# Kernel tuning notes

Measured on AMD Instinct MI355X. Metric: run time of the kernel, lower is better.

Reference implementation:

```python
import jax, jax.numpy as jnp
import numpy as np

N_NODES = 9
NEG_SLOPE = 0.2
# static edge list from the module (src, dst) pairs, PyG convention row0=src, row1=dst
_E = np.array([[0,1],[1,0],[0,3],[3,0],[0,5],[5,0],[0,7],[7,0],
               [1,2],[2,1],[3,4],[4,3],[5,6],[6,5],[7,8],[8,7]], dtype=np.int32).T
# GATv2Conv default add_self_loops=True
SRC = jnp.asarray(np.concatenate([_E[0], np.arange(N_NODES, dtype=np.int32)]))
DST = jnp.asarray(np.concatenate([_E[1], np.arange(N_NODES, dtype=np.int32)]))


def setup_inputs() -> dict:
    key = jax.random.key(0)
    k1, k2, k3, k4 = jax.random.split(key, 4)
    B, C_IN, C_OUT = 16384, 256, 256
    scale = 1.0 / np.sqrt(C_IN)
    return {
        "x": jax.random.normal(k1, (B, N_NODES, C_IN), jnp.float32),
        "W_l": jax.random.normal(k2, (C_IN, C_OUT), jnp.float32) * scale,
        "W_r": jax.random.normal(k3, (C_IN, C_OUT), jnp.float32) * scale,
        "att": jax.random.normal(k4, (C_OUT,), jnp.float32) * scale,
        "bias": jnp.zeros((C_OUT,), jnp.float32),
    }


def reference(x, W_l, W_r, att, bias):
    # x: [B, N, C_in] batch of identical small graphs
    xl = jnp.einsum("bnc,cd->bnd", x, W_l)  # source-side projection
    xr = jnp.einsum("bnc,cd->bnd", x, W_r)  # target-side projection
    # per-edge GATv2 score: a^T LeakyReLU(x_l[src] + x_r[dst])
    e = jax.nn.leaky_relu(xl[:, SRC] + xr[:, DST], NEG_SLOPE)  # [B, E, C_out]
    score = jnp.einsum("bed,d->be", e, att)                    # [B, E]
    # softmax over incoming edges of each destination node (segment softmax)
    sT = score.T                                               # [E, B]
    m = jax.ops.segment_max(sT, DST, num_segments=N_NODES)     # [N, B]
    ex = jnp.exp(sT - m[DST])
    denom = jax.ops.segment_sum(ex, DST, num_segments=N_NODES)
    alpha = ex / denom[DST]                                    # [E, B]
    # scatter-aggregate messages alpha * x_l[src] into dst
    msg = xl[:, SRC] * alpha.T[..., None]                      # [B, E, C_out]
    out = jax.ops.segment_sum(msg.transpose(1, 0, 2), DST, num_segments=N_NODES)
    return out.transpose(1, 0, 2) + bias                       # [B, N, C_out]
```

## Files before the change

### kernel.cpp

```cpp
#include <hip/hip_runtime.h>
#include <hip/hip_bf16.h>

typedef __attribute__((ext_vector_type(8))) short short8;
typedef __attribute__((ext_vector_type(4))) float f32x4;
typedef __attribute__((ext_vector_type(4))) unsigned short u16x4;

#define STAGE_BYTES (144 * 512)
#define PART_OFF    0
#define ALPHA_OFF   (8 * 25 * 16 * 4)
#define LDS_BYTES   STAGE_BYTES

__device__ __forceinline__ unsigned short f2bf(float f) {
    unsigned int u = __float_as_uint(f);
    unsigned int r = (u + 0x7fffu + ((u >> 16) & 1u)) >> 16;
    return (unsigned short)r;
}

constexpr int C_SRC[25] = {0,1,0,3,0,5,0,7,1,2,3,4,5,6,7,8, 0,1,2,3,4,5,6,7,8};
constexpr int C_DST[25] = {1,0,3,0,5,0,7,0,2,1,4,3,6,5,8,7, 0,1,2,3,4,5,6,7,8};
constexpr int C_NINC[9]  = {5,3,2,3,2,3,2,3,2};
constexpr int C_IOFF[9]  = {0,5,8,10,13,15,18,20,23};
constexpr int C_INCE[25] = {1,3,5,7,16, 0,9,17, 8,18, 2,11,19, 10,20, 4,13,21, 12,22, 6,15,23, 14,24};
constexpr int C_INCS[25] = {1,3,5,7,0,  0,2,1,  1,2,  0,4,3,  3,4,  0,6,5,  5,6,  0,8,7,  7,8};
__device__ const int D_NINC[9]  = {5,3,2,3,2,3,2,3,2};
__device__ const int D_IOFF[9]  = {0,5,8,10,13,15,18,20,23};
__device__ const int D_INCE[25] = {1,3,5,7,16, 0,9,17, 8,18, 2,11,19, 10,20, 4,13,21, 12,22, 6,15,23, 14,24};

__global__ void convert_w_kernel(const float* __restrict__ Wl,
                                 const float* __restrict__ Wr,
                                 unsigned short* __restrict__ WT) {
    int n = blockIdx.x;
    int k = threadIdx.x;
    float v = (n < 256) ? Wl[k * 256 + n] : Wr[k * 256 + (n - 256)];
    WT[n * 256 + k] = f2bf(v);
}

__global__ __launch_bounds__(512, 2) void gat_fused_kernel(
        const float* __restrict__ x,
        const unsigned short* __restrict__ WT,
        const float* __restrict__ att,
        const float* __restrict__ bias,
        float* __restrict__ out) {
    __shared__ __align__(16) char smem[LDS_BYTES];
    float* partials = (float*)(smem + PART_OFF);
    float* alphas   = (float*)(smem + ALPHA_OFF);

    const int tid  = threadIdx.x;
    const int lane = tid & 63;
    const int w    = tid >> 6;
    const int gl   = lane >> 4;
    const int li   = lane & 15;
    const int blk  = blockIdx.x;

    const int c0 = 32 * w + li, c1 = c0 + 16;
    const float attc0 = att[c0], attc1 = att[c1];
    const float bc0   = bias[c0], bc1 = bias[c1];

    const float* xblk = x + (size_t)blk * 36864;
    {
        f32x4 xv[18];
        #pragma unroll
        for (int it = 0; it < 18; ++it)
            xv[it] = *(const f32x4*)(xblk + it * 2048 + tid * 4);
        #pragma unroll
        for (int it = 0; it < 18; ++it) {
            int f    = it * 2048 + tid * 4;
            int gr   = f >> 8;
            int c    = f & 255;
            int g    = gr / 9;
            int node = gr - g * 9;
            int srow = node * 16 + g;
            u16x4 pk = { f2bf(xv[it][0]), f2bf(xv[it][1]), f2bf(xv[it][2]), f2bf(xv[it][3]) };
            *(u16x4*)(smem + srow * 512 + ((2 * c) ^ (g << 4))) = pk;
        }
    }
    __syncthreads();

    const f32x4 ZERO = {0.f, 0.f, 0.f, 0.f};
    f32x4 aL[9][2], aR[9][2];
    #pragma unroll
    for (int m = 0; m < 9; ++m) {
        aL[m][0] = ZERO; aL[m][1] = ZERO; aR[m][0] = ZERO; aR[m][1] = ZERO;
    }
    const unsigned short* WL0 = WT + (size_t)((32 * w + li) * 256 + gl * 8);
    const unsigned short* WL1 = WL0 + 16 * 256;
    const unsigned short* WR0 = WL0 + 256 * 256;
    const unsigned short* WR1 = WR0 + 16 * 256;

    #pragma unroll
    for (int kc = 0; kc < 8; ++kc) {
        short8 bl0 = *(const short8*)(WL0 + kc * 32);
        short8 bl1 = *(const short8*)(WL1 + kc * 32);
        short8 br0 = *(const short8*)(WR0 + kc * 32);
        short8 br1 = *(const short8*)(WR1 + kc * 32);
        const int inner = ((kc * 64) + (gl * 16)) ^ (li << 4);
        short8 am[9];
        #pragma unroll
        for (int m = 0; m < 9; ++m)
            am[m] = *(const short8*)(smem + (m * 16 + li) * 512 + inner);
        #pragma unroll
        for (int m = 0; m < 9; ++m) {
            aL[m][0] = __builtin_amdgcn_mfma_f32_16x16x32_bf16(am[m], bl0, aL[m][0], 0, 0, 0);
            aL[m][1] = __builtin_amdgcn_mfma_f32_16x16x32_bf16(am[m], bl1, aL[m][1], 0, 0, 0);
            aR[m][0] = __builtin_amdgcn_mfma_f32_16x16x32_bf16(am[m], br0, aR[m][0], 0, 0, 0);
            aR[m][1] = __builtin_amdgcn_mfma_f32_16x16x32_bf16(am[m], br1, aR[m][1], 0, 0, 0);
        }
    }
    __syncthreads();

    #pragma unroll
    for (int e = 0; e < 25; ++e) {
        const int s = C_SRC[e], d = C_DST[e];
        float p0 = 0.f, p1 = 0.f, p2 = 0.f, p3 = 0.f;
        #pragma unroll
        for (int nt = 0; nt < 2; ++nt) {
            const float ac = nt ? attc1 : attc0;
            #pragma unroll
            for (int r = 0; r < 4; ++r) {
                float v  = aL[s][nt][r] + aR[d][nt][r];
                float lr = fmaxf(v, 0.2f * v);
                float t  = ac * lr;
                if (r == 0) p0 += t; else if (r == 1) p1 += t;
                else if (r == 2) p2 += t; else p3 += t;
            }
        }
        #pragma unroll
        for (int m = 1; m < 16; m <<= 1) {
            p0 += __shfl_xor(p0, m);
            p1 += __shfl_xor(p1, m);
            p2 += __shfl_xor(p2, m);
            p3 += __shfl_xor(p3, m);
        }
        if (li == 0) {
            f32x4 pk = {p0, p1, p2, p3};
            *(f32x4*)(partials + (w * 25 + e) * 16 + 4 * gl) = pk;
        }
    }
    __syncthreads();

    if (tid < 144) {
        int n = tid >> 4, g = tid & 15;
        int off = D_IOFF[n], cnt = D_NINC[n];
        float mx = -1e30f;
        for (int i = 0; i < cnt; ++i) {
            int e = D_INCE[off + i];
            float s = 0.f;
            #pragma unroll
            for (int ww = 0; ww < 8; ++ww) s += partials[(ww * 25 + e) * 16 + g];
            alphas[e * 16 + g] = s;
            mx = fmaxf(mx, s);
        }
        float ssum = 0.f;
        for (int i = 0; i < cnt; ++i)
            ssum += __expf(alphas[D_INCE[off + i] * 16 + g] - mx);
        float inv = 1.f / ssum;
        for (int i = 0; i < cnt; ++i) {
            int e = D_INCE[off + i];
            alphas[e * 16 + g] = __expf(alphas[e * 16 + g] - mx) * inv;
        }
    }
    __syncthreads();

    #pragma unroll
    for (int n = 0; n < 9; ++n) {
        f32x4 o0 = {bc0, bc0, bc0, bc0};
        f32x4 o1 = {bc1, bc1, bc1, bc1};
        #pragma unroll
        for (int i = 0; i < C_NINC[n]; ++i) {
            const int e  = C_INCE[C_IOFF[n] + i];
            const int sn = C_INCS[C_IOFF[n] + i];
            f32x4 al = *(const f32x4*)(alphas + e * 16 + 4 * gl);
            #pragma unroll
            for (int r = 0; r < 4; ++r) {
                o0[r] += al[r] * aL[sn][0][r];
                o1[r] += al[r] * aL[sn][1][r];
            }
        }
        #pragma unroll
        for (int r = 0; r < 4; ++r) {
            size_t row = (size_t)(blk * 16 + 4 * gl + r) * 9 + n;
            out[row * 256 + c0] = o0[r];
            out[row * 256 + c1] = o1[r];
        }
    }
}

extern "C" void kernel_launch(void* const* d_in, const int* in_sizes, int n_in,
                              void* d_out, int out_size, void* d_ws, size_t ws_size,
                              hipStream_t stream) {
    const float* x    = (const float*)d_in[0];
    const float* Wl   = (const float*)d_in[1];
    const float* Wr   = (const float*)d_in[2];
    const float* att  = (const float*)d_in[3];
    const float* bias = (const float*)d_in[4];
    float* out = (float*)d_out;
    unsigned short* WT = (unsigned short*)d_ws;

    convert_w_kernel<<<512, 256, 0, stream>>>(Wl, Wr, WT);
    gat_fused_kernel<<<1024, 512, 0, stream>>>(x, WT, att, bias, out);
}
```

Baseline: 140.9 us.

## Pre-convert x to swizzled bf16 and double-buffer LDS loads in persistent blocks

Adds a separate kernel that converts x to bf16 in the swizzled LDS layout and writes it to workspace. The main kernel then runs 256 blocks that each process 4 units, prefetching the next unit into a second LDS buffer with global_load_lds while the current unit is computed. This is meant to hide global-load latency and take the conversion off the critical path. In exchange it adds an extra full pass that writes and rereads a bf16 copy of x, doubles the LDS footprint, which may lower occupancy, and launches only 256 blocks. The old fused kernel is kept as a fallback when the workspace is too small.

```diff
diff --git a/kernel.cpp b/kernel.cpp
--- a/kernel.cpp
+++ b/kernel.cpp
@@ -5,15 +5,27 @@
 typedef __attribute__((ext_vector_type(4))) float f32x4;
 typedef __attribute__((ext_vector_type(4))) unsigned short u16x4;
 
-#define STAGE_BYTES (144 * 512)
-#define PART_OFF    0
-#define ALPHA_OFF   (8 * 25 * 16 * 4)
-#define LDS_BYTES   STAGE_BYTES
+#define STAGE_BYTES 73728
+#define NU 4
+#define PART_OFF  (2 * STAGE_BYTES)
+#define ALPHA_OFF (PART_OFF + 8 * 25 * 16 * 4)
+#define MAIN_LDS  (ALPHA_OFF + 25 * 16 * 4)
+
+#define WT_BYTES   (512 * 256 * 2)
+#define XPRE_BYTES (1024 * STAGE_BYTES)
+#define WS_NEED    ((size_t)WT_BYTES + (size_t)XPRE_BYTES)
 
 __device__ __forceinline__ unsigned short f2bf(float f) {
     unsigned int u = __float_as_uint(f);
     unsigned int r = (u + 0x7fffu + ((u >> 16) & 1u)) >> 16;
     return (unsigned short)r;
+}
+
+__device__ __forceinline__ void gload_lds16(const unsigned char* g, unsigned char* l) {
+    __builtin_amdgcn_global_load_lds(
+        (const __attribute__((address_space(1))) unsigned int*)g,
+        (__attribute__((address_space(3))) unsigned int*)l,
+        16, 0, 0);
 }
 
 constexpr int C_SRC[25] = {0,1,0,3,0,5,0,7,1,2,3,4,5,6,7,8, 0,1,2,3,4,5,6,7,8};
@@ -35,15 +47,189 @@
     WT[n * 256 + k] = f2bf(v);
 }
 
-__global__ __launch_bounds__(512, 2) void gat_fused_kernel(
+__global__ __launch_bounds__(512) void cvt_x_kernel(const float* __restrict__ x,
+                                                    unsigned char* __restrict__ xp) {
+    const int u = blockIdx.x;
+    const int t = threadIdx.x;
+    const float* xu = x + (size_t)u * 36864;
+    unsigned char* xpu = xp + (size_t)u * STAGE_BYTES;
+    #pragma unroll
+    for (int it = 0; it < 9; ++it) {
+        int ci   = it * 512 + t;
+        int srow = ci >> 5;
+        int g    = srow & 15, node = srow >> 4;
+        int ib   = (ci & 31) * 16;
+        int cb   = (ib ^ (g << 4)) >> 1;
+        const float* src = xu + ((size_t)g * 9 + node) * 256 + cb;
+        f32x4 a = *(const f32x4*)(src);
+        f32x4 b = *(const f32x4*)(src + 4);
+        u16x4 lo = { f2bf(a[0]), f2bf(a[1]), f2bf(a[2]), f2bf(a[3]) };
+        u16x4 hi = { f2bf(b[0]), f2bf(b[1]), f2bf(b[2]), f2bf(b[3]) };
+        *(u16x4*)(xpu + ci * 16)     = lo;
+        *(u16x4*)(xpu + ci * 16 + 8) = hi;
+    }
+}
+
+__global__ __launch_bounds__(512, 2) void gat_main_kernel(
+        const unsigned char* __restrict__ xp,
+        const unsigned short* __restrict__ WT,
+        const float* __restrict__ att,
+        const float* __restrict__ bias,
+        float* __restrict__ out) {
+    __shared__ __align__(16) unsigned char smem[MAIN_LDS];
+    float* partials = (float*)(smem + PART_OFF);
+    float* alphas   = (float*)(smem + ALPHA_OFF);
+
+    const int tid  = threadIdx.x;
+    const int lane = tid & 63;
+    const int w    = tid >> 6;
+    const int gl   = lane >> 4;
+    const int li   = lane & 15;
+    const int c0 = 32 * w + li, c1 = c0 + 16;
+    const float attc0 = att[c0], attc1 = att[c1];
+    const float bc0   = bias[c0], bc1 = bias[c1];
+
+    const unsigned short* WL = WT + (size_t)(c0 * 256 + gl * 8);
+    const unsigned short* WR = WL + 256 * 256;
+    const f32x4 ZERO = {0.f, 0.f, 0.f, 0.f};
+    const size_t unit0 = (size_t)blockIdx.x * NU;
+
+    {
+        const unsigned char* src = xp + unit0 * STAGE_BYTES;
+        #pragma unroll
+        for (int j = 0; j < 9; ++j)
+            gload_lds16(src + ((w * 9 + j) << 10) + lane * 16, smem + ((w * 9 + j) << 10));
+    }
+    __syncthreads();
+
+    int cur = 0;
+    for (int u = 0; u < NU; ++u) {
+        unsigned char* bufc = smem + cur * STAGE_BYTES;
+        unsigned char* bufn = smem + (cur ^ 1) * STAGE_BYTES;
+
+        if (u + 1 < NU) {
+            const unsigned char* src = xp + (unit0 + u + 1) * STAGE_BYTES;
+            #pragma unroll
+            for (int j = 0; j < 9; ++j)
+                gload_lds16(src + ((w * 9 + j) << 10) + lane * 16, bufn + ((w * 9 + j) << 10));
+        }
+
+        f32x4 aL[9][2], aR[9][2];
+        #pragma unroll
+        for (int m = 0; m < 9; ++m) {
+            aL[m][0] = ZERO; aL[m][1] = ZERO; aR[m][0] = ZERO; aR[m][1] = ZERO;
+        }
+        #pragma unroll
+        for (int kc = 0; kc < 8; ++kc) {
+            short8 bl0 = *(const short8*)(WL + kc * 32);
+            short8 bl1 = *(const short8*)(WL + 16 * 256 + kc * 32);
+            short8 br0 = *(const short8*)(WR + kc * 32);
+            short8 br1 = *(const short8*)(WR + 16 * 256 + kc * 32);
+            const int inner = ((kc * 64) + (gl * 16)) ^ (li << 4);
+            short8 am[9];
+            #pragma unroll
+            for (int m = 0; m < 9; ++m)
+                am[m] = *(const short8*)(bufc + (m * 16 + li) * 512 + inner);
+            #pragma unroll
+            for (int m = 0; m < 9; ++m) {
+                aL[m][0] = __builtin_amdgcn_mfma_f32_16x16x32_bf16(am[m], bl0, aL[m][0], 0, 0, 0);
+                aL[m][1] = __builtin_amdgcn_mfma_f32_16x16x32_bf16(am[m], bl1, aL[m][1], 0, 0, 0);
+                aR[m][0] = __builtin_amdgcn_mfma_f32_16x16x32_bf16(am[m], br0, aR[m][0], 0, 0, 0);
+                aR[m][1] = __builtin_amdgcn_mfma_f32_16x16x32_bf16(am[m], br1, aR[m][1], 0, 0, 0);
+            }
+        }
+
+        #pragma unroll
+        for (int e = 0; e < 25; ++e) {
+            const int s = C_SRC[e], d = C_DST[e];
+            float p0 = 0.f, p1 = 0.f, p2 = 0.f, p3 = 0.f;
+            #pragma unroll
+            for (int nt = 0; nt < 2; ++nt) {
+                const float ac = nt ? attc1 : attc0;
+                #pragma unroll
+                for (int r = 0; r < 4; ++r) {
+                    float v  = aL[s][nt][r] + aR[d][nt][r];
+                    float lr = fmaxf(v, 0.2f * v);
+                    float t  = ac * lr;
+                    if (r == 0) p0 += t; else if (r == 1) p1 += t;
+                    else if (r == 2) p2 += t; else p3 += t;
+                }
+            }
+            #pragma unroll
+            for (int m = 1; m < 16; m <<= 1) {
+                p0 += __shfl_xor(p0, m);
+                p1 += __shfl_xor(p1, m);
+                p2 += __shfl_xor(p2, m);
+                p3 += __shfl_xor(p3, m);
+            }
+            if (li == 0) {
+                f32x4 pk = {p0, p1, p2, p3};
+                *(f32x4*)(partials + (w * 25 + e) * 16 + 4 * gl) = pk;
+            }
+        }
+        __syncthreads();
+
+        if (tid < 144) {
+            int n = tid >> 4, g = tid & 15;
+            int off = D_IOFF[n], cnt = D_NINC[n];
+            float mx = -1e30f;
+            for (int i = 0; i < cnt; ++i) {
+                int e = D_INCE[off + i];
+                float s = 0.f;
+                #pragma unroll
+                for (int ww = 0; ww < 8; ++ww) s += partials[(ww * 25 + e) * 16 + g];
+                alphas[e * 16 + g] = s;
+                mx = fmaxf(mx, s);
+            }
+            float ssum = 0.f;
+            for (int i = 0; i < cnt; ++i)
+                ssum += __expf(alphas[D_INCE[off + i] * 16 + g] - mx);
+            float inv = 1.f / ssum;
+            for (int i = 0; i < cnt; ++i) {
+                int e = D_INCE[off + i];
+                alphas[e * 16 + g] = __expf(alphas[e * 16 + g] - mx) * inv;
+            }
+        }
+        __syncthreads();
+
+        float* outblk = out + (unit0 + u) * 36864;
+        #pragma unroll
+        for (int n = 0; n < 9; ++n) {
+            f32x4 o0 = {bc0, bc0, bc0, bc0};
+            f32x4 o1 = {bc1, bc1, bc1, bc1};
+            #pragma unroll
+            for (int i = 0; i < C_NINC[n]; ++i) {
+                const int e  = C_INCE[C_IOFF[n] + i];
+                const int sn = C_INCS[C_IOFF[n] + i];
+                f32x4 al = *(const f32x4*)(alphas + e * 16 + 4 * gl);
+                #pragma unroll
+                for (int r = 0; r < 4; ++r) {
+                    o0[r] += al[r] * aL[sn][0][r];
+                    o1[r] += al[r] * aL[sn][1][r];
+                }
+            }
+            #pragma unroll
+            for (int r = 0; r < 4; ++r) {
+                int row = (4 * gl + r) * 9 + n;
+                outblk[row * 256 + c0] = o0[r];
+                outblk[row * 256 + c1] = o1[r];
+            }
+        }
+        cur ^= 1;
+    }
+}
+
+#define L_PART_OFF  0
+#define L_ALPHA_OFF (8 * 25 * 16 * 4)
+__global__ __launch_bounds__(512, 2) void gat_fused_legacy(
         const float* __restrict__ x,
         const unsigned short* __restrict__ WT,
         const float* __restrict__ att,
         const float* __restrict__ bias,
         float* __restrict__ out) {
-    __shared__ __align__(16) char smem[LDS_BYTES];
-    float* partials = (float*)(smem + PART_OFF);
-    float* alphas   = (float*)(smem + ALPHA_OFF);
+    __shared__ __align__(16) char smem[STAGE_BYTES];
+    float* partials = (float*)(smem + L_PART_OFF);
+    float* alphas   = (float*)(smem + L_ALPHA_OFF);
 
     const int tid  = threadIdx.x;
     const int lane = tid & 63;
@@ -51,7 +237,6 @@
     const int gl   = lane >> 4;
     const int li   = lane & 15;
     const int blk  = blockIdx.x;
-
     const int c0 = 32 * w + li, c1 = c0 + 16;
     const float attc0 = att[c0], attc1 = att[c1];
     const float bc0   = bias[c0], bc1 = bias[c1];
@@ -76,23 +261,20 @@
     }
     __syncthreads();
 
+    const unsigned short* WL = WT + (size_t)(c0 * 256 + gl * 8);
+    const unsigned short* WR = WL + 256 * 256;
     const f32x4 ZERO = {0.f, 0.f, 0.f, 0.f};
     f32x4 aL[9][2], aR[9][2];
     #pragma unroll
     for (int m = 0; m < 9; ++m) {
         aL[m][0] = ZERO; aL[m][1] = ZERO; aR[m][0] = ZERO; aR[m][1] = ZERO;
     }
-    const unsigned short* WL0 = WT + (size_t)((32 * w + li) * 256 + gl * 8);
-    const unsigned short* WL1 = WL0 + 16 * 256;
-    const unsigned short* WR0 = WL0 + 256 * 256;
-    const unsigned short* WR1 = WR0 + 16 * 256;
-
     #pragma unroll
     for (int kc = 0; kc < 8; ++kc) {
-        short8 bl0 = *(const short8*)(WL0 + kc * 32);
-        short8 bl1 = *(const short8*)(WL1 + kc * 32);
-        short8 br0 = *(const short8*)(WR0 + kc * 32);
-        short8 br1 = *(const short8*)(WR1 + kc * 32);
+        short8 bl0 = *(const short8*)(WL + kc * 32);
+        short8 bl1 = *(const short8*)(WL + 16 * 256 + kc * 32);
+        short8 br0 = *(const short8*)(WR + kc * 32);
+        short8 br1 = *(const short8*)(WR + 16 * 256 + kc * 32);
         const int inner = ((kc * 64) + (gl * 16)) ^ (li << 4);
         short8 am[9];
         #pragma unroll
@@ -197,5 +379,11 @@
     unsigned short* WT = (unsigned short*)d_ws;
 
     convert_w_kernel<<<512, 256, 0, stream>>>(Wl, Wr, WT);
-    gat_fused_kernel<<<1024, 512, 0, stream>>>(x, WT, att, bias, out);
-}
+    if (ws_size >= WS_NEED) {
+        unsigned char* xp = (unsigned char*)d_ws + WT_BYTES;
+        cvt_x_kernel<<<1024, 512, 0, stream>>>(x, xp);
+        gat_main_kernel<<<256, 512, 0, stream>>>(xp, WT, att, bias, out);
+    } else {
+        gat_fused_legacy<<<1024, 512, 0, stream>>>(x, WT, att, bias, out);
+    }
+}
```

Result: slower. 337.6 us (+139.7%).
